# Performance work log

Hardware: AMD Instinct MI355X
Metric: run time of the kernel (lower is better)

The kernel has to match this reference:

```python
import jax, jax.numpy as jnp
import numpy as np
import math

B, T, D = 2, 512, 1024
H, HD = 16, 64
F = 4096
L = 2
R = 32
LOOP_DIM = 64
TEMB = 256
MAXIT = 8
TOPK = 0.55
EPS = 1e-6


def _ste(x, q):
    # straight-through estimator: forward = q, backward = identity
    return x + jax.lax.stop_gradient(q - x)


def bitlinear(x, w, topk_ratio=None):
    # BitNet b1.58 fake-quant: ternary weights (per-tensor absmean scale),
    # int8 per-token absmax activations; optional topk activation sparsity.
    s = jnp.mean(jnp.abs(w)) + 1e-8
    wq = _ste(w, jnp.clip(jnp.round(w / s), -1.0, 1.0) * s)
    if topk_ratio is not None:
        k = max(1, int(math.ceil(topk_ratio * x.shape[-1])))
        ax = jnp.abs(x)
        thr = jax.lax.top_k(ax, k)[0][..., -1:]
        x = jnp.where(ax >= thr, x, 0.0)
    a = jnp.maximum(jnp.max(jnp.abs(x), axis=-1, keepdims=True), 1e-8)
    xq = _ste(x, jnp.clip(jnp.round(x * (127.0 / a)), -128.0, 127.0) * (a / 127.0))
    return xq @ wq.T


def rmsnorm(x, w):
    return x * jax.lax.rsqrt(jnp.mean(x * x, axis=-1, keepdims=True) + EPS) * w


def _rope(x):
    # x: (B,H,T,HD)
    half = HD // 2
    inv = 1.0 / (10000.0 ** (jnp.arange(half, dtype=jnp.float32) / half))
    ang = jnp.arange(x.shape[2], dtype=jnp.float32)[:, None] * inv[None, :]
    cos, sin = jnp.cos(ang), jnp.sin(ang)
    x1, x2 = x[..., :half], x[..., half:]
    return jnp.concatenate([x1 * cos - x2 * sin, x1 * sin + x2 * cos], axis=-1)


def bitblock(h, n1, wq, wk, wv, wo, n2, wg, wu, wd):
    # pre-norm attention + SwiGLU FFN, all projections BitLinear
    b, t, _ = h.shape
    a_in = rmsnorm(h, n1)
    heads = lambda p: p.reshape(b, t, H, HD).transpose(0, 2, 1, 3)
    q = _rope(heads(bitlinear(a_in, wq)))
    k = _rope(heads(bitlinear(a_in, wk)))
    v = heads(bitlinear(a_in, wv))
    scores = jnp.einsum('bhqd,bhkd->bhqk', q, k) / math.sqrt(HD)
    mask = jnp.tril(jnp.ones((t, t), dtype=bool))
    attn = jax.nn.softmax(jnp.where(mask, scores, -1e9), axis=-1)
    o = jnp.einsum('bhqk,bhkd->bhqd', attn, v).transpose(0, 2, 1, 3).reshape(b, t, D)
    h = h + bitlinear(o, wo)
    f_in = rmsnorm(h, n2)
    h = h + bitlinear(jax.nn.silu(bitlinear(f_in, wg)) * bitlinear(f_in, wu), wd)
    return h


def loop_delta(i, t_emb, lp_w, lp2_w, lp2_b):
    # loop_index_inject: sinusoidal loop signal gated by t_emb, padded to D
    half = LOOP_DIM // 2
    frac = i / max(MAXIT - 1, 1)
    freqs = jnp.exp(-math.log(10000.0) * jnp.arange(half, dtype=jnp.float32) / half)
    ang = frac * freqs
    sig = jnp.concatenate([jnp.sin(ang), jnp.cos(ang)])  # (LOOP_DIM,)
    comb = sig[None, :] * (t_emb @ lp_w.T) + (t_emb @ lp2_w.T + lp2_b)  # (B,LOOP_DIM)
    return jnp.pad(comb, ((0, 0), (0, D - LOOP_DIM)))[:, None, :]  # (B,1,D)


def setup_inputs() -> dict:
    key = jax.random.key(0)
    ks = jax.random.split(key, 24)
    g = lambda k, shape, sc=0.02: sc * jax.random.normal(k, shape, dtype=jnp.float32)
    return {
        'x': jax.random.normal(ks[0], (B, T, D), dtype=jnp.float32),
        'e': jax.random.normal(ks[1], (B, T, D), dtype=jnp.float32),
        't_emb': jax.random.normal(ks[2], (B, TEMB), dtype=jnp.float32),
        'blk_norm1': jnp.ones((L, D), jnp.float32),
        'blk_wq': g(ks[3], (L, D, D)),
        'blk_wk': g(ks[4], (L, D, D)),
        'blk_wv': g(ks[5], (L, D, D)),
        'blk_wo': g(ks[6], (L, D, D)),
        'blk_norm2': jnp.ones((L, D), jnp.float32),
        'blk_wg': g(ks[7], (L, F, D)),
        'blk_wu': g(ks[8], (L, F, D)),
        'blk_wd': g(ks[9], (L, D, F)),
        'A_raw': 0.1 * jax.random.normal(ks[10], (D,), dtype=jnp.float32),
        'B_w': g(ks[11], (D, D)),
        'lora_down': g(ks[12], (R, D)),
        'lora_up': g(ks[13], (D, R)),
        'iter_gate': jnp.full((MAXIT,), 0.1, jnp.float32),
        'act_w': g(ks[14], (1, D)),
        'alpha': jnp.full((MAXIT,), 1.0 / L, jnp.float32),
        'loop_proj_w': g(ks[15], (LOOP_DIM, TEMB)),
        'loop_proj2_w': g(ks[16], (LOOP_DIM, TEMB)),
        'loop_proj2_b': jnp.zeros((LOOP_DIM,), jnp.float32),
        'loop_norm_w': jnp.ones((D,), jnp.float32),
        'n_loops': 8,
    }


def reference(x, e, t_emb, blk_norm1, blk_wq, blk_wk, blk_wv, blk_wo,
              blk_norm2, blk_wg, blk_wu, blk_wd, A_raw, B_w,
              lora_down, lora_up, iter_gate, act_w, alpha,
              loop_proj_w, loop_proj2_w, loop_proj2_b, loop_norm_w, n_loops):
    A_eff = 0.99 * jnp.tanh(A_raw)          # diagonal LTI, |A|<0.99
    Be = bitlinear(e, B_w)                  # loop-invariant anchor B(e)
    h = x
    h_out = x
    ws = []
    for i in range(int(n_loops)):
        h_in = rmsnorm(h + loop_delta(i, t_emb, loop_proj_w, loop_proj2_w, loop_proj2_b), loop_norm_w)
        bo = h_in
        for l in range(L):
            bo = bitblock(bo, blk_norm1[l], blk_wq[l], blk_wk[l], blk_wv[l], blk_wo[l],
                          blk_norm2[l], blk_wg[l], blk_wu[l], blk_wd[l])
        bo = alpha[i] * bo
        h = A_eff * h + Be + bo             # LTI injection
        h = h + iter_gate[i] * bitlinear(bitlinear(h, lora_down), lora_up, topk_ratio=TOPK)
        w = jax.nn.sigmoid(bitlinear(h, act_w))  # (B,T,1) soft ACT weight
        h_out = h_out + w * (h - h_out)     # incremental residual blend
        ws.append(w)
    ponder = jnp.mean(jnp.stack(ws))
    return h_out, ponder
```

## Files before the change

### kernel.cpp

```cpp
#include <hip/hip_runtime.h>
#include <stdint.h>

#define DEV static __device__ __forceinline__

typedef float f32x4 __attribute__((ext_vector_type(4)));
typedef int   i32x4 __attribute__((ext_vector_type(4)));
typedef unsigned short u16x8 __attribute__((ext_vector_type(8)));

DEV float bf2f(unsigned short u){ return __uint_as_float(((unsigned int)u)<<16); }
DEV unsigned short f2bfr(float f){
  unsigned int u = __float_as_uint(f);
  return (unsigned short)((u + 0x7FFF + ((u>>16)&1)) >> 16);
}
DEV signed char f2i8(float f){ return (signed char)(int)f; }

DEV float wredsum(float v){
#pragma unroll
  for (int o=32;o;o>>=1) v += __shfl_xor(v,o);
  return v;
}
DEV float wredmax(float v){
#pragma unroll
  for (int o=32;o;o>>=1) v = fmaxf(v,__shfl_xor(v,o));
  return v;
// ... 12 lines not shown
  __syncthreads();
  float r = fmaxf(fmaxf(red[0],red[1]),fmaxf(red[2],red[3]));
  __syncthreads();
  return r;
}

__global__ void fill_k(float* p, int n, float v){
  int i = blockIdx.x*256 + threadIdx.x;
  if (i < n) p[i] = v;
}

__global__ __launch_bounds__(256) void copy_init_k(const float* __restrict__ x,
                                                   float* __restrict__ h, float* __restrict__ ho){
  int i = blockIdx.x*256 + threadIdx.x;
  float4 v = *(const float4*)(x + (size_t)i*4);
  *(float4*)(h  + (size_t)i*4) = v;
  *(float4*)(ho + (size_t)i*4) = v;
  if (blockIdx.x==0 && threadIdx.x==0) ho[1048576] = 0.f;
}

struct WSetup {
  const float* src[18];
  signed char* dst[18];
};
DEV long n4of(int mat){ return mat<9 ? 262144 : (mat<15 ? 1048576 : (mat<17 ? 8192 : 256)); }

__global__ __launch_bounds__(256) void absmean_all_k(WSetup wsu, float* __restrict__ part){
  __shared__ float red[4];
  int mat = blockIdx.x >> 8;
  int seg = blockIdx.x & 255;
  long n4 = n4of(mat);
  const float4* p = (const float4*)wsu.src[mat];
  float s0=0.f, s1=0.f, s2=0.f, s3=0.f;
  long i = (long)seg*256 + threadIdx.x;
  for (; i + 196608 < n4; i += 262144){
    float4 a = p[i], b = p[i+65536], c = p[i+131072], d = p[i+196608];
    s0 += fabsf(a.x)+fabsf(a.y)+fabsf(a.z)+fabsf(a.w);
    s1 += fabsf(b.x)+fabsf(b.y)+fabsf(b.z)+fabsf(b.w);
    s2 += fabsf(c.x)+fabsf(c.y)+fabsf(c.z)+fabsf(c.w);
    s3 += fabsf(d.x)+fabsf(d.y)+fabsf(d.z)+fabsf(d.w);
  }
  for (; i < n4; i += 65536){
    float4 a = p[i];
    s0 += fabsf(a.x)+fabsf(a.y)+fabsf(a.z)+fabsf(a.w);
  }
  float s = bredsum(s0+s1+s2+s3, red);
  if (threadIdx.x==0) part[(long)mat*256 + seg] = s;
}

__global__ __launch_bounds__(256) void finalize_scales_k(const float* __restrict__ part,
                                                         float* __restrict__ scales){
  __shared__ float red[4];
  const long numel[18] = {1048576, 1048576,1048576, 1048576,1048576, 1048576,1048576,
                          1048576,1048576, 4194304,4194304, 4194304,4194304, 4194304,4194304,
                          32768, 32768, 1024};
  for (int m=0;m<18;m++){
    float v = part[(long)m*256 + threadIdx.x];
    v = bredsum(v, red);
    if (threadIdx.x==0) scales[m] = v/(float)numel[m] + 1e-8f;
  }
  if (threadIdx.x==0){
    for (int l=0;l<2;l++){
      scales[18+l*3+0] = scales[1+l];
      scales[18+l*3+1] = scales[3+l];
      scales[18+l*3+2] = scales[5+l];
      scales[24+l*2+0] = scales[9+l];
      scales[24+l*2+1] = scales[11+l];
    }
  }
}

__global__ __launch_bounds__(256) void quantw_all_k(WSetup wsu, const float* __restrict__ scales){
  int bid = blockIdx.x;
  int mat = 0, c = 0;
  for (;;){
    int nb = mat<9 ? 256 : (mat<15 ? 1024 : (mat<17 ? 8 : 1));
    if (bid < c + nb) break;
    c += nb; mat++;
  }
  long seg = bid - c;
  long n4 = n4of(mat);
  float s = scales[mat];
  const float4* src = (const float4*)wsu.src[mat];
  char4* dst = (char4*)wsu.dst[mat];
  long base = seg*1024;
#pragma unroll
  for (int k=0;k<4;k++){
    long i = base + k*256 + threadIdx.x;
    if (i < n4){
      float4 v = src[i];
      char4 q;
      q.x = f2i8(fminf(fmaxf(rintf(v.x/s), -1.f), 1.f));
      q.y = f2i8(fminf(fmaxf(rintf(v.y/s), -1.f), 1.f));
      q.z = f2i8(fminf(fmaxf(rintf(v.z/s), -1.f), 1.f));
      q.w = f2i8(fminf(fmaxf(rintf(v.w/s), -1.f), 1.f));
      dst[i] = q;
    }
  }
}

__global__ __launch_bounds__(256) void delta2_k(const float* __restrict__ temb,
                                                const float* __restrict__ lpw,
                                                const float* __restrict__ lp2w,
                                                const float* __restrict__ lp2b,
                                                float* __restrict__ delta){
  __shared__ float red[4];
  int blk = blockIdx.x;
  int b = blk >> 6, j = blk & 63;
  int t = threadIdx.x;
  float te = temb[b*256 + t];
  float p1 = bredsum(te * lpw[j*256 + t], red);
  float p2 = bredsum(te * lp2w[j*256 + t], red);
  if (t < 8){
    int i = t;
    float frac = (float)i / 7.f;
    int jj = j & 31;
    float fr = expf(-logf(10000.f) * (float)jj * (1.f/32.f));
    float ang = frac * fr;
    float sig = (j < 32) ? sinf(ang) : cosf(ang);
// ... 10 lines not shown
  tab[i*2+1] = sv;
}

__global__ __launch_bounds__(256) void rowquant1k_k(const float* __restrict__ x,
                                                    signed char* __restrict__ xq,
                                                    float* __restrict__ rs){
  __shared__ float red[4];
  int m = blockIdx.x, t = threadIdx.x;
  float v[4];
  float4 f = *(const float4*)(x + (size_t)m*1024 + t*4);
  v[0]=f.x; v[1]=f.y; v[2]=f.z; v[3]=f.w;
  float am = fmaxf(fmaxf(fabsf(v[0]),fabsf(v[1])),fmaxf(fabsf(v[2]),fabsf(v[3])));
  am = bredmax(am, red);
  float a = fmaxf(am, 1e-8f), inv = 127.f/a;
  char4 q;
  q.x = f2i8(fminf(fmaxf(rintf(v[0]*inv),-128.f),127.f));
  q.y = f2i8(fminf(fmaxf(rintf(v[1]*inv),-128.f),127.f));
  q.z = f2i8(fminf(fmaxf(rintf(v[2]*inv),-128.f),127.f));
  q.w = f2i8(fminf(fmaxf(rintf(v[3]*inv),-128.f),127.f));
  *(char4*)(xq + (size_t)m*1024 + t*4) = q;
  if (t==0) rs[m] = a/127.f;
}

__global__ __launch_bounds__(256) void loopnorm_quant_k(const float* __restrict__ h,
                                                        const float* __restrict__ delta,
                                                        const float* __restrict__ lnw,
                                                        const float* __restrict__ n1,
                                                        float* __restrict__ hin,
                                                        signed char* __restrict__ xq,
                                                        float* __restrict__ rs){
  __shared__ float red[4];
  int m = blockIdx.x, t = threadIdx.x;
  int b = m >> 9;
  float v[4];
  float4 f = *(const float4*)(h + (size_t)m*1024 + t*4);
  v[0]=f.x; v[1]=f.y; v[2]=f.z; v[3]=f.w;
  if (t < 16){
#pragma unroll
    for (int j=0;j<4;j++) v[j] += delta[b*64 + t*4 + j];
  }
  float ss = v[0]*v[0]+v[1]*v[1]+v[2]*v[2]+v[3]*v[3];
  ss = bredsum(ss, red);
  float r1 = rsqrtf(ss*(1.f/1024.f) + 1e-6f);
  float w4[4];
#pragma unroll
  for (int j=0;j<4;j++) w4[j] = v[j]*r1*lnw[t*4+j];
  float4 of; of.x=w4[0]; of.y=w4[1]; of.z=w4[2]; of.w=w4[3];
  *(float4*)(hin + (size_t)m*1024 + t*4) = of;
  float s2 = w4[0]*w4[0]+w4[1]*w4[1]+w4[2]*w4[2]+w4[3]*w4[3];
  s2 = bredsum(s2, red);
  float r2 = rsqrtf(s2*(1.f/1024.f) + 1e-6f);
  float y[4];
#pragma unroll
  for (int j=0;j<4;j++) y[j] = w4[j]*r2*n1[t*4+j];
  float am = fmaxf(fmaxf(fabsf(y[0]),fabsf(y[1])),fmaxf(fabsf(y[2]),fabsf(y[3])));
  am = bredmax(am, red);
  float a = fmaxf(am, 1e-8f), inv = 127.f/a;
  char4 q;
  q.x = f2i8(fminf(fmaxf(rintf(y[0]*inv),-128.f),127.f));
  q.y = f2i8(fminf(fmaxf(rintf(y[1]*inv),-128.f),127.f));
  q.z = f2i8(fminf(fmaxf(rintf(y[2]*inv),-128.f),127.f));
  q.w = f2i8(fminf(fmaxf(rintf(y[3]*inv),-128.f),127.f));
  *(char4*)(xq + (size_t)m*1024 + t*4) = q;
  if (t==0) rs[m] = a/127.f;
}

__global__ __launch_bounds__(256) void silu_mul_quant_k(const float* __restrict__ gu,
                                                        signed char* __restrict__ xq,
                                                        float* __restrict__ rs){
  __shared__ float red[4];
  int m = blockIdx.x, t = threadIdx.x;
  const float* g = gu + (size_t)m*8192;
  const float* u = g + 4096;
  float v[16];
#pragma unroll
  for (int j=0;j<16;j+=4){
    float4 gg = *(const float4*)(g + t*16 + j);
    float4 uu = *(const float4*)(u + t*16 + j);
    v[j+0] = gg.x/(1.f+expf(-gg.x))*uu.x;
    v[j+1] = gg.y/(1.f+expf(-gg.y))*uu.y;
    v[j+2] = gg.z/(1.f+expf(-gg.z))*uu.z;
    v[j+3] = gg.w/(1.f+expf(-gg.w))*uu.w;
  }
  float am = 0.f;
#pragma unroll
  for (int j=0;j<16;j++) am = fmaxf(am, fabsf(v[j]));
  am = bredmax(am, red);
  float a = fmaxf(am, 1e-8f), inv = 127.f/a;
#pragma unroll
  for (int j=0;j<16;j+=4){
    char4 q;
    q.x = f2i8(fminf(fmaxf(rintf(v[j+0]*inv),-128.f),127.f));
    q.y = f2i8(fminf(fmaxf(rintf(v[j+1]*inv),-128.f),127.f));
    q.z = f2i8(fminf(fmaxf(rintf(v[j+2]*inv),-128.f),127.f));
    q.w = f2i8(fminf(fmaxf(rintf(v[j+3]*inv),-128.f),127.f));
    *(char4*)(xq + (size_t)m*4096 + t*16 + j) = q;
  }
  if (t==0) rs[m] = a/127.f;
}

DEV f32x4 accfence(f32x4 c){ asm volatile("s_nop 7\n\ts_nop 7" : "+v"(c)); return c; }
DEV i32x4 accfencei(i32x4 c){ asm volatile("s_nop 7\n\ts_nop 7" : "+v"(c)); return c; }

template<int SSHIFT, bool SPLITK>
__global__ __launch_bounds__(256)
void gemm_i8(const signed char* __restrict__ A, const signed char* __restrict__ W,
             const float* __restrict__ rowsc, const float* __restrict__ wscv,
             const float* __restrict__ res, float* __restrict__ C, int N, int Kf, int Kc)
{
  __shared__ __align__(16) signed char As[2][8192];
  __shared__ __align__(16) signed char Bs[2][8192];
  const int tid = threadIdx.x;
  const int lane = tid & 63, wvid = tid >> 6;
  const int wr = wvid >> 1, wc = wvid & 1;
  const int bm = blockIdx.y, bn = blockIdx.x;

  const int r0 = (wvid<<4) + (lane>>2);
  const int sw = (((lane&3) ^ ((r0>>1)&3)) << 4);
  const long kstart = SPLITK ? (long)blockIdx.z * Kc : 0;
  const signed char* gA = A + (size_t)(bm*128 + r0)*Kf + kstart + sw;
  const signed char* gB = W + (size_t)(bn*128 + r0)*Kf + kstart + sw;
  const size_t row64 = (size_t)64*Kf;

#define STAGE(buf, koff) do { \
    __builtin_amdgcn_global_load_lds(gA + (koff),         &As[buf][(wvid<<10)],      16, 0, 0); \
    __builtin_amdgcn_global_load_lds(gA + (koff) + row64, &As[buf][(wvid<<10)+4096], 16, 0, 0); \
    __builtin_amdgcn_global_load_lds(gB + (koff),         &Bs[buf][(wvid<<10)],      16, 0, 0); \
// ... 36 lines not shown
  for (int mi=0;mi<4;mi++)
#pragma unroll
    for (int ni=0;ni<4;ni++)
      acc[mi][ni] = accfencei(acc[mi][ni]);

  const int rif = (lane>>4)<<2;
  const int cif = lane&15;
  const int gcol0 = bn*128 + (wc<<6);

  if constexpr (SPLITK){
    float* P = C + (size_t)blockIdx.z * ((size_t)N << 10);
#pragma unroll
    for (int mi=0;mi<4;mi++)
#pragma unroll
      for (int r=0;r<4;r++){
        const int grow = bm*128 + (wr<<6) + mi*16 + rif + r;
#pragma unroll
        for (int ni=0;ni<4;ni++)
          P[(size_t)grow*N + gcol0 + ni*16 + cif] = (float)acc[mi][ni][r];
      }
    return;
  }

#pragma unroll
  for (int mi=0;mi<4;mi++){
#pragma unroll
    for (int r=0;r<4;r++){
      const int grow = bm*128 + (wr<<6) + mi*16 + rif + r;
      const float rsc = rowsc[grow];
#pragma unroll
      for (int ni=0;ni<4;ni++){
        const int gcol = gcol0 + ni*16 + cif;
        float vvv = (float)acc[mi][ni][r] * rsc * wscv[gcol>>SSHIFT];
        const size_t off = (size_t)grow*N + gcol;
        if (res) vvv += res[off];
        C[off] = vvv;
      }
    }
  }
}

__global__ __launch_bounds__(256) void rope_reduce_k(const float* P,
                                                     const float* __restrict__ rowsc,
                                                     const float* __restrict__ wscv,
                                                     const float* __restrict__ tab,
                                                     float* C){
  int m = blockIdx.x, t = threadIdx.x;
  const float rsc = rowsc[m];
  const int tpos = m & 511;
  const size_t base = (size_t)m*3072;
  const float* P1 = P + 3145728;
  int p0 = t*4;
  int hh = p0 >> 5, d = p0 & 31;
  int c1 = hh*64 + d;
  float wsc = wscv[c1>>10] * rsc;
  float4 xa0 = *(const float4*)(P  + base + c1);
  float4 xa1 = *(const float4*)(P1 + base + c1);
  float4 xb0 = *(const float4*)(P  + base + c1 + 32);
  float4 xb1 = *(const float4*)(P1 + base + c1 + 32);
  float4 cs01 = *(const float4*)(tab + ((size_t)tpos*32 + d)*2);
  float4 cs23 = *(const float4*)(tab + ((size_t)tpos*32 + d)*2 + 4);
  int cv = 2048 + t*4;
  float4 va = *(const float4*)(P  + base + cv);
  float4 vb = *(const float4*)(P1 + base + cv);
  float wv2 = wscv[2] * rsc;

  float x1[4] = {(xa0.x+xa1.x)*wsc, (xa0.y+xa1.y)*wsc, (xa0.z+xa1.z)*wsc, (xa0.w+xa1.w)*wsc};
  float x2[4] = {(xb0.x+xb1.x)*wsc, (xb0.y+xb1.y)*wsc, (xb0.z+xb1.z)*wsc, (xb0.w+xb1.w)*wsc};
  float cc[4] = {cs01.x, cs01.z, cs23.x, cs23.z};
  float ss[4] = {cs01.y, cs01.w, cs23.y, cs23.w};
  float4 o1, o2, ov;
  o1.x = x1[0]*cc[0] - x2[0]*ss[0];  o2.x = x1[0]*ss[0] + x2[0]*cc[0];
  o1.y = x1[1]*cc[1] - x2[1]*ss[1];  o2.y = x1[1]*ss[1] + x2[1]*cc[1];
  o1.z = x1[2]*cc[2] - x2[2]*ss[2];  o2.z = x1[2]*ss[2] + x2[2]*cc[2];
  o1.w = x1[3]*cc[3] - x2[3]*ss[3];  o2.w = x1[3]*ss[3] + x2[3]*cc[3];
  ov.x = (va.x+vb.x)*wv2; ov.y = (va.y+vb.y)*wv2; ov.z = (va.z+vb.z)*wv2; ov.w = (va.w+vb.w)*wv2;
  *(float4*)(C + base + c1)      = o1;
  *(float4*)(C + base + c1 + 32) = o2;
  *(float4*)(C + base + cv)      = ov;
}

__global__ __launch_bounds__(256) void reduce4_k(const float* __restrict__ P,
                                                 const float* __restrict__ rowsc,
                                                 const float* __restrict__ wsc,
                                                 const float* __restrict__ res,
                                                 float* __restrict__ C){
  int m = blockIdx.x, t = threadIdx.x;
  float s0 = rowsc[m] * wsc[0];
  size_t off = (size_t)m*1024 + t*4;
  float4 a = *(const float4*)(P + off);
  float4 b = *(const float4*)(P + 1048576 + off);
  float4 c = *(const float4*)(P + 2097152 + off);
  float4 d = *(const float4*)(P + 3145728 + off);
  float4 o;
  o.x = (a.x+b.x+c.x+d.x)*s0;
  o.y = (a.y+b.y+c.y+d.y)*s0;
  o.z = (a.z+b.z+c.z+d.z)*s0;
  o.w = (a.w+b.w+c.w+d.w)*s0;
  if (res){
    float4 r = *(const float4*)(res + off);
    o.x += r.x; o.y += r.y; o.z += r.z; o.w += r.w;
  }
// ... 38 lines not shown
  q.y = f2i8(fminf(fmaxf(rintf(y[1]*inv),-128.f),127.f));
  q.z = f2i8(fminf(fmaxf(rintf(y[2]*inv),-128.f),127.f));
  q.w = f2i8(fminf(fmaxf(rintf(y[3]*inv),-128.f),127.f));
  *(char4*)(xq + (size_t)m*1024 + t*4) = q;
  if (t==0) rs[m] = aq/127.f;
}

__global__ __launch_bounds__(256) void redfin_k(const float* __restrict__ P,
                                                const float* __restrict__ rowsc,
                                                const float* __restrict__ wsc,
                                                const float* __restrict__ res,
                                                float* __restrict__ h,
                                                const float* __restrict__ Be,
                                                const float* __restrict__ Araw,
                                                const float* __restrict__ alpha, int it,
                                                const signed char* __restrict__ ldq,
                                                const float* __restrict__ sld,
                                                const signed char* __restrict__ luq,
                                                const float* __restrict__ slu,
                                                const signed char* __restrict__ actq,
                                                const float* __restrict__ sact,
                                                const float* __restrict__ ig,
                                                float* __restrict__ hout,
                                                float* __restrict__ ponder){
  __shared__ float red[4];
  __shared__ float xrow[1024];
  __shared__ float part[256];
  __shared__ float xs[32];
  __shared__ float sh_thr, sh_gs;
  int m = blockIdx.x, t = threadIdx.x;
  float al = alpha[it];
  float s0 = rowsc[m] * wsc[0];
  size_t off = (size_t)m*1024 + t*4;
  float4 a = *(const float4*)(P + off);
  float4 b = *(const float4*)(P + 1048576 + off);
  float4 c = *(const float4*)(P + 2097152 + off);
  float4 d = *(const float4*)(P + 3145728 + off);
  float4 r4 = *(const float4*)(res + off);
  float4 hh = *(const float4*)(h + off);
  float4 be = *(const float4*)(Be + off);
  float4 ar = *(const float4*)(Araw + t*4);
  float v[4];
  v[0] = 0.99f*tanhf(ar.x)*hh.x + be.x + al*(r4.x + (a.x+b.x+c.x+d.x)*s0);
  v[1] = 0.99f*tanhf(ar.y)*hh.y + be.y + al*(r4.y + (a.y+b.y+c.y+d.y)*s0);
  v[2] = 0.99f*tanhf(ar.z)*hh.z + be.z + al*(r4.z + (a.z+b.z+c.z+d.z)*s0);
  v[3] = 0.99f*tanhf(ar.w)*hh.w + be.w + al*(r4.w + (a.w+b.w+c.w+d.w)*s0);
  float am = fmaxf(fmaxf(fabsf(v[0]),fabsf(v[1])),fmaxf(fabsf(v[2]),fabsf(v[3])));
// ... 54 lines not shown
    }
    hn[ni] = v[ni] + gs*dd;
  }
  float am2 = fmaxf(fmaxf(fabsf(hn[0]),fabsf(hn[1])),fmaxf(fabsf(hn[2]),fabsf(hn[3])));
  am2 = bredmax(am2, red);
  float a2 = fmaxf(am2, 1e-8f), inv2 = 127.f/a2;
  float zp = 0.f;
#pragma unroll
  for (int ni=0;ni<4;ni++){
    float q = fminf(fmaxf(rintf(hn[ni]*inv2),-128.f),127.f);
    zp += q * (float)actq[n0+ni];
  }
  zp = bredsum(zp, red);
  float z = zp * (a2/127.f) * (*sact);
  float wv = 1.f/(1.f+expf(-z));
#pragma unroll
  for (int ni=0;ni<4;ni++){
    size_t o2 = (size_t)m*1024 + n0+ni;
    float ho = hout[o2];
    hout[o2] = ho + wv*(hn[ni]-ho);
    h[o2] = hn[ni];
  }
  if (t==0) atomicAdd(ponder, wv * (1.f/8192.f));
}

DEV int swz64(int r, int c){ return r*64 + (c ^ ((r&7)<<3)); }
DEV u16x8 cvt8(float4 a, float4 b, float sc){
  u16x8 q;
  q[0]=f2bfr(a.x*sc); q[1]=f2bfr(a.y*sc); q[2]=f2bfr(a.z*sc); q[3]=f2bfr(a.w*sc);
  q[4]=f2bfr(b.x*sc); q[5]=f2bfr(b.y*sc); q[6]=f2bfr(b.z*sc); q[7]=f2bfr(b.w*sc);
  return q;
}

__global__ __launch_bounds__(256) void attn_mfma_k(const float* __restrict__ qkv,
                                                   float* __restrict__ o){
  __shared__ __align__(16) unsigned short Qs[4096];
  __shared__ __align__(16) unsigned short Ks[4096];
  __shared__ __align__(16) unsigned short Vt[4096];
  __shared__ __align__(16) unsigned short Ps[4][1024];
  const int tid = threadIdx.x;
  const int lane = tid & 63, wv = tid >> 6;
  const int qt = blockIdx.x & 7, bh = blockIdx.x >> 3;
  const int b = bh >> 4, h = bh & 15;
  const size_t tokbase = (size_t)(b*512);
  const int l15 = lane & 15, lh = lane >> 4;

  {
    int r = tid >> 2, c0 = (tid & 3) << 4;
    const float* s = qkv + (tokbase + qt*64 + r)*3072 + h*64 + c0;
    float4 f0 = *(const float4*)s,     f1 = *(const float4*)(s+4);
    float4 f2 = *(const float4*)(s+8), f3 = *(const float4*)(s+12);
    *(u16x8*)(Qs + swz64(r, c0))   = cvt8(f0, f1, 0.125f);
    *(u16x8*)(Qs + swz64(r, c0+8)) = cvt8(f2, f3, 0.125f);
  }

  float m_run[4] = {-1e30f,-1e30f,-1e30f,-1e30f};
  float l_run[4] = {0.f,0.f,0.f,0.f};
  f32x4 accO[4] = {};

  for (int kt = 0; kt <= qt; ++kt){
    __syncthreads();
    {
      int r = tid >> 2, c0 = (tid & 3) << 4;
      const float* s = qkv + (tokbase + kt*64 + r)*3072 + 1024 + h*64 + c0;
      float4 f0 = *(const float4*)s,     f1 = *(const float4*)(s+4);
      float4 f2 = *(const float4*)(s+8), f3 = *(const float4*)(s+12);
      *(u16x8*)(Ks + swz64(r, c0))   = cvt8(f0, f1, 1.f);
      *(u16x8*)(Ks + swz64(r, c0+8)) = cvt8(f2, f3, 1.f);
    }
    {
      int r0 = (tid >> 3) << 1, cv = (tid & 7) << 3;
      const float* s0 = qkv + (tokbase + kt*64 + r0)*3072 + 2048 + h*64 + cv;
      const float* s1 = s0 + 3072;
      float4 a0 = *(const float4*)s0, a1 = *(const float4*)(s0+4);
      float4 b0 = *(const float4*)s1, b1 = *(const float4*)(s1+4);
      float va[8] = {a0.x,a0.y,a0.z,a0.w,a1.x,a1.y,a1.z,a1.w};
      float vb[8] = {b0.x,b0.y,b0.z,b0.w,b1.x,b1.y,b1.z,b1.w};
#pragma unroll
      for (int j=0;j<8;j++){
        int d = cv + j;
        unsigned int pk = (unsigned int)f2bfr(va[j]) | ((unsigned int)f2bfr(vb[j])<<16);
        *(unsigned int*)(Vt + swz64(d, r0)) = pk;
      }
    }
    __syncthreads();

    f32x4 s4[4] = {};
#pragma unroll
    for (int kc=0; kc<2; ++kc){
      i32x4 aq = *(const i32x4*)(Qs + swz64(wv*16 + l15, kc*32 + lh*8));
#pragma unroll
      for (int nt=0; nt<4; ++nt){
        i32x4 bk = *(const i32x4*)(Ks + swz64(nt*16 + l15, kc*32 + lh*8));
        asm("v_mfma_f32_16x16x32_bf16 %0, %1, %2, %0" : "+v"(s4[nt]) : "v"(aq), "v"(bk));
      }
    }
#pragma unroll
    for (int nt=0; nt<4; ++nt) s4[nt] = accfence(s4[nt]);

    const bool diag = (kt == qt);
    float sf[4];
#pragma unroll
    for (int r=0;r<4;r++){
      int rl = lh*4 + r;
// ... 14 lines not shown
      m_run[r] = mn;
      float ps = 0.f;
#pragma unroll
      for (int nt=0; nt<4; ++nt){
        float p = __expf(s4[nt][r] - mn);
        ps += p;
        Ps[wv][swz64(rl, nt*16 + l15)] = f2bfr(p);
      }
      ps += __shfl_xor(ps,1); ps += __shfl_xor(ps,2);
      ps += __shfl_xor(ps,4); ps += __shfl_xor(ps,8);
      l_run[r] = l_run[r]*sf[r] + ps;
    }
#pragma unroll
    for (int dt=0; dt<4; ++dt){
#pragma unroll
      for (int r=0;r<4;r++) accO[dt][r] *= sf[r];
      accO[dt] = accfence(accO[dt]);
    }
#pragma unroll
    for (int kc=0; kc<2; ++kc){
      i32x4 pa = *(const i32x4*)(Ps[wv] + swz64(l15, kc*32 + lh*8));
#pragma unroll
      for (int dt=0; dt<4; ++dt){
        i32x4 vb2 = *(const i32x4*)(Vt + swz64(dt*16 + l15, kc*32 + lh*8));
        asm("v_mfma_f32_16x16x32_bf16 %0, %1, %2, %0" : "+v"(accO[dt]) : "v"(pa), "v"(vb2));
      }
    }
  }
#pragma unroll
  for (int dt=0; dt<4; ++dt) accO[dt] = accfence(accO[dt]);
#pragma unroll
  for (int r=0;r<4;r++){
    float invl = 1.f / l_run[r];
    int row = qt*64 + wv*16 + lh*4 + r;
    float* op = o + (tokbase + row)*1024 + h*64 + l15;
#pragma unroll
    for (int dt=0; dt<4; ++dt)
      op[dt*16] = accO[dt][r] * invl;
  }
}

extern "C" void kernel_launch(void* const* d_in, const int* in_sizes, int n_in,
                              void* d_out, int out_size, void* d_ws, size_t ws_size,
                              hipStream_t stream)
{
  (void)in_sizes; (void)n_in;
  const float* x     = (const float*)d_in[0];
  const float* e     = (const float*)d_in[1];
  const float* temb  = (const float*)d_in[2];
  const float* bn1   = (const float*)d_in[3];
  const float* bwq   = (const float*)d_in[4];
  const float* bwk   = (const float*)d_in[5];
  const float* bwv   = (const float*)d_in[6];
  const float* bwo   = (const float*)d_in[7];
  const float* bn2   = (const float*)d_in[8];
  const float* bwg   = (const float*)d_in[9];
  const float* bwu   = (const float*)d_in[10];
  const float* bwd   = (const float*)d_in[11];
// ... 13 lines not shown
  float* out = (float*)d_out;
  const size_t WS_NEEDED = 94600704ull;
  if (ws_size < WS_NEEDED){
    fill_k<<<(out_size+255)/256,256,0,stream>>>(out, out_size, 1.0e9f);
    return;
  }

  signed char* qw_qkv = (signed char*)(ws + 0);
  signed char* qw_wo  = (signed char*)(ws + 6291456);
  signed char* qw_gu  = (signed char*)(ws + 8388608);
  signed char* qw_wd  = (signed char*)(ws + 25165824);
  signed char* qw_bw  = (signed char*)(ws + 33554432);
  signed char* qw_ld  = (signed char*)(ws + 34603008);
  signed char* qw_lu  = (signed char*)(ws + 34635776);
  signed char* qw_act = (signed char*)(ws + 34668544);
  float* scales = (float*)(ws + 34669568);
  float* part   = (float*)(ws + 34670080);
  float* delta  = (float*)(ws + 34688512);
  float* hbuf   = (float*)(ws + 34692608);
  float* Bebuf  = (float*)(ws + 38886912);
  float* bufX   = (float*)(ws + 43081216);
  float* bufY   = (float*)(ws + 47275520);
  float* gub    = (float*)(ws + 51469824);
  float* qkvb   = gub;
  float* obuf   = (float*)(ws + 85024256);
  signed char* xq1k = (signed char*)(ws + 89218560);
  float* rs1k   = (float*)(ws + 90267136);
  signed char* xqm  = (signed char*)(ws + 90271232);
  float* rsm    = (float*)(ws + 94465536);
  float* ropetab= (float*)(ws + 94469632);

  WSetup wsu;
  wsu.src[0]=Bw;
  wsu.src[1]=bwq; wsu.src[2]=bwq+1048576;
  wsu.src[3]=bwk; wsu.src[4]=bwk+1048576;
  wsu.src[5]=bwv; wsu.src[6]=bwv+1048576;
  wsu.src[7]=bwo; wsu.src[8]=bwo+1048576;
  wsu.src[9]=bwg; wsu.src[10]=bwg+4194304;
  wsu.src[11]=bwu; wsu.src[12]=bwu+4194304;
  wsu.src[13]=bwd; wsu.src[14]=bwd+4194304;
  wsu.src[15]=ldw; wsu.src[16]=luw; wsu.src[17]=actw;
  wsu.dst[0]=qw_bw;
  wsu.dst[1]=qw_qkv;             wsu.dst[2]=qw_qkv+3145728;
  wsu.dst[3]=qw_qkv+1048576;     wsu.dst[4]=qw_qkv+3145728+1048576;
  wsu.dst[5]=qw_qkv+2097152;     wsu.dst[6]=qw_qkv+3145728+2097152;
  wsu.dst[7]=qw_wo;              wsu.dst[8]=qw_wo+1048576;
  wsu.dst[9]=qw_gu;              wsu.dst[10]=qw_gu+8388608;
  wsu.dst[11]=qw_gu+4194304;     wsu.dst[12]=qw_gu+8388608+4194304;
  wsu.dst[13]=qw_wd;             wsu.dst[14]=qw_wd+4194304;
  wsu.dst[15]=qw_ld; wsu.dst[16]=qw_lu; wsu.dst[17]=qw_act;

  absmean_all_k<<<4608,256,0,stream>>>(wsu, part);
  finalize_scales_k<<<1,256,0,stream>>>(part, scales);
  quantw_all_k<<<8465,256,0,stream>>>(wsu, scales);

  delta2_k<<<128,256,0,stream>>>(temb, lpw, lp2w, lp2b, delta);
  ropetab_k<<<64,256,0,stream>>>(ropetab);
  copy_init_k<<<1024,256,0,stream>>>(x, hbuf, out);

  rowquant1k_k<<<1024,256,0,stream>>>(e, xq1k, rs1k);
  { dim3 g(8,8,4); gemm_i8<0,true><<<g,256,0,stream>>>(xq1k, qw_bw, nullptr, nullptr, nullptr, gub, 1024, 1024, 256); }
  reduce4_k<<<1024,256,0,stream>>>(gub, rs1k, scales+0, nullptr, Bebuf);

  for (int it=0; it<8; ++it){
    loopnorm_quant_k<<<1024,256,0,stream>>>(hbuf, delta + it*128, lnw, bn1, bufX, xq1k, rs1k);
    for (int l=0;l<2;l++){
      { dim3 g(24,8,2); gemm_i8<0,true><<<g,256,0,stream>>>(xq1k, qw_qkv + (size_t)l*3145728, nullptr, nullptr, nullptr, gub, 3072, 1024, 512); }
      rope_reduce_k<<<1024,256,0,stream>>>(gub, rs1k, scales+18+l*3, ropetab, qkvb);
      attn_mfma_k<<<256,256,0,stream>>>(qkvb, obuf);
      rowquant1k_k<<<1024,256,0,stream>>>(obuf, xq1k, rs1k);
      { dim3 g(8,8,4); gemm_i8<0,true><<<g,256,0,stream>>>(xq1k, qw_wo + (size_t)l*1048576, nullptr, nullptr, nullptr, gub, 1024, 1024, 256); }
      redq_norm_k<<<1024,256,0,stream>>>(gub, rs1k, scales+7+l, bufX, bn2 + (size_t)l*1024, bufY, xq1k, rs1k);
      { dim3 g(64,8); gemm_i8<12,false><<<g,256,0,stream>>>(xq1k, qw_gu + (size_t)l*8388608, rs1k, scales+24+l*2, nullptr, gub, 8192, 1024, 1024); }
      silu_mul_quant_k<<<1024,256,0,stream>>>(gub, xqm, rsm);
      { dim3 g(8,8,4); gemm_i8<0,true><<<g,256,0,stream>>>(xqm, qw_wd + (size_t)l*4194304, nullptr, nullptr, nullptr, gub, 1024, 4096, 1024); }
      if (l==0){
        redq_norm_k<<<1024,256,0,stream>>>(gub, rsm, scales+13, bufY, bn1 + 1024, bufX, xq1k, rs1k);
      } else {
        redfin_k<<<1024,256,0,stream>>>(gub, rsm, scales+14, bufY, hbuf, Bebuf, Araw, alph, it,
                                        qw_ld, scales+15, qw_lu, scales+16, qw_act, scales+17,
                                        ig, out, out + 1048576);
      }
    }
  }
}
```

Baseline: 2.111 ms.

## Fuse RoPE into attention, SiLU into gate/up GEMM, loopnorm into final reduce

Fuses RoPE and the split-K reduction into the attention kernel, so the separate rope_reduce pass and its intermediate buffer disappear. The gate and up weights are interleaved row by row so the gate/up GEMM epilogue can apply SiLU times up via a lane shuffle, writing a 4096-wide result that only needs row quantisation. The next iteration's loop-norm and quantisation are fused into the tail of redfin_k, and the absmean reduction now reads contiguous segments per block. Together these cut launches and global memory round trips, at the cost of extra per-element work in the attention load phase and a half-lane store pattern in the GEMM epilogue.

Result: slower. 2.243 ms (+6.3%).

```diff
diff --git a/kernel.cpp b/kernel.cpp
--- a/kernel.cpp
+++ b/kernel.cpp
@@ -58,6 +58,7 @@
 struct WSetup {
   const float* src[18];
   signed char* dst[18];
+  int mode[18];
 };
 DEV long n4of(int mat){ return mat<9 ? 262144 : (mat<15 ? 1048576 : (mat<17 ? 8192 : 256)); }
 
@@ -66,18 +67,19 @@
   int mat = blockIdx.x >> 8;
   int seg = blockIdx.x & 255;
   long n4 = n4of(mat);
-  const float4* p = (const float4*)wsu.src[mat];
+  long cnt = n4 >> 8;
+  const float4* p = (const float4*)wsu.src[mat] + (long)seg*cnt;
   float s0=0.f, s1=0.f, s2=0.f, s3=0.f;
-  long i = (long)seg*256 + threadIdx.x;
-  for (; i + 196608 < n4; i += 262144){
-    float4 a = p[i], b = p[i+65536], c = p[i+131072], d = p[i+196608];
+  long j = threadIdx.x;
+  for (; j + 768 < cnt; j += 1024){
+    float4 a = p[j], b = p[j+256], c = p[j+512], d = p[j+768];
     s0 += fabsf(a.x)+fabsf(a.y)+fabsf(a.z)+fabsf(a.w);
     s1 += fabsf(b.x)+fabsf(b.y)+fabsf(b.z)+fabsf(b.w);
     s2 += fabsf(c.x)+fabsf(c.y)+fabsf(c.z)+fabsf(c.w);
     s3 += fabsf(d.x)+fabsf(d.y)+fabsf(d.z)+fabsf(d.w);
   }
-  for (; i < n4; i += 65536){
-    float4 a = p[i];
+  for (; j < cnt; j += 256){
+    float4 a = p[j];
     s0 += fabsf(a.x)+fabsf(a.y)+fabsf(a.z)+fabsf(a.w);
   }
   float s = bredsum(s0+s1+s2+s3, red);
@@ -117,6 +119,7 @@
   long seg = bid - c;
   long n4 = n4of(mat);
   float s = scales[mat];
+  int md = wsu.mode[mat];
   const float4* src = (const float4*)wsu.src[mat];
   char4* dst = (char4*)wsu.dst[mat];
   long base = seg*1024;
@@ -130,7 +133,11 @@
       q.y = f2i8(fminf(fmaxf(rintf(v.y/s), -1.f), 1.f));
       q.z = f2i8(fminf(fmaxf(rintf(v.z/s), -1.f), 1.f));
       q.w = f2i8(fminf(fmaxf(rintf(v.w/s), -1.f), 1.f));
-      dst[i] = q;
+      if (md == 0) dst[i] = q;
+      else {
+        long r = i >> 8, cc = i & 255;
+        dst[(((r<<1) | (md-1))<<8) | cc] = q;
+      }
     }
   }
 }
@@ -187,6 +194,35 @@
   if (t==0) rs[m] = a/127.f;
 }
 
+__global__ __launch_bounds__(256) void rowquant4k_k(const float* __restrict__ x,
+                                                    signed char* __restrict__ xq,
+                                                    float* __restrict__ rs){
+  __shared__ float red[4];
+  int m = blockIdx.x, t = threadIdx.x;
+  const float* p = x + (size_t)m*4096 + t*16;
+  float v[16];
+#pragma unroll
+  for (int j=0;j<16;j+=4){
+    float4 f = *(const float4*)(p + j);
+    v[j]=f.x; v[j+1]=f.y; v[j+2]=f.z; v[j+3]=f.w;
+  }
+  float am = 0.f;
+#pragma unroll
+  for (int j=0;j<16;j++) am = fmaxf(am, fabsf(v[j]));
+  am = bredmax(am, red);
+  float a = fmaxf(am, 1e-8f), inv = 127.f/a;
+#pragma unroll
+  for (int j=0;j<16;j+=4){
+    char4 q;
+    q.x = f2i8(fminf(fmaxf(rintf(v[j+0]*inv),-128.f),127.f));
+    q.y = f2i8(fminf(fmaxf(rintf(v[j+1]*inv),-128.f),127.f));
+    q.z = f2i8(fminf(fmaxf(rintf(v[j+2]*inv),-128.f),127.f));
+    q.w = f2i8(fminf(fmaxf(rintf(v[j+3]*inv),-128.f),127.f));
+    *(char4*)(xq + (size_t)m*4096 + t*16 + j) = q;
+  }
+  if (t==0) rs[m] = a/127.f;
+}
+
 __global__ __launch_bounds__(256) void loopnorm_quant_k(const float* __restrict__ h,
                                                         const float* __restrict__ delta,
                                                         const float* __restrict__ lnw,
@@ -230,44 +266,10 @@
   if (t==0) rs[m] = a/127.f;
 }
 
-__global__ __launch_bounds__(256) void silu_mul_quant_k(const float* __restrict__ gu,
-                                                        signed char* __restrict__ xq,
-                                                        float* __restrict__ rs){
-  __shared__ float red[4];
-  int m = blockIdx.x, t = threadIdx.x;
-  const float* g = gu + (size_t)m*8192;
-  const float* u = g + 4096;
-  float v[16];
-#pragma unroll
-  for (int j=0;j<16;j+=4){
-    float4 gg = *(const float4*)(g + t*16 + j);
-    float4 uu = *(const float4*)(u + t*16 + j);
-    v[j+0] = gg.x/(1.f+expf(-gg.x))*uu.x;
-    v[j+1] = gg.y/(1.f+expf(-gg.y))*uu.y;
-    v[j+2] = gg.z/(1.f+expf(-gg.z))*uu.z;
-    v[j+3] = gg.w/(1.f+expf(-gg.w))*uu.w;
-  }
-  float am = 0.f;
-#pragma unroll
-  for (int j=0;j<16;j++) am = fmaxf(am, fabsf(v[j]));
-  am = bredmax(am, red);
-  float a = fmaxf(am, 1e-8f), inv = 127.f/a;
-#pragma unroll
-  for (int j=0;j<16;j+=4){
-    char4 q;
-    q.x = f2i8(fminf(fmaxf(rintf(v[j+0]*inv),-128.f),127.f));
-    q.y = f2i8(fminf(fmaxf(rintf(v[j+1]*inv),-128.f),127.f));
-    q.z = f2i8(fminf(fmaxf(rintf(v[j+2]*inv),-128.f),127.f));
-    q.w = f2i8(fminf(fmaxf(rintf(v[j+3]*inv),-128.f),127.f));
-    *(char4*)(xq + (size_t)m*4096 + t*16 + j) = q;
-  }
-  if (t==0) rs[m] = a/127.f;
-}
-
 DEV f32x4 accfence(f32x4 c){ asm volatile("s_nop 7\n\ts_nop 7" : "+v"(c)); return c; }
 DEV i32x4 accfencei(i32x4 c){ asm volatile("s_nop 7\n\ts_nop 7" : "+v"(c)); return c; }
 
-template<int SSHIFT, bool SPLITK>
+template<bool SPLITK, bool GUSILU>
 __global__ __launch_bounds__(256)
 void gemm_i8(const signed char* __restrict__ A, const signed char* __restrict__ W,
              const float* __restrict__ rowsc, const float* __restrict__ wscv,
@@ -350,6 +352,30 @@
     return;
   }
 
+  if constexpr (GUSILU){
+    const float sg = wscv[0], su = wscv[1];
+#pragma unroll
+    for (int mi=0;mi<4;mi++){
+#pragma unroll
+      for (int r=0;r<4;r++){
+        const int grow = bm*128 + (wr<<6) + mi*16 + rif + r;
+        const float rsc = rowsc[grow];
+#pragma unroll
+        for (int ni=0;ni<4;ni++){
+          const int gcol = gcol0 + ni*16 + cif;
+          float val = (float)acc[mi][ni][r] * rsc * ((gcol & 1) ? su : sg);
+          float other = __shfl_xor(val, 1);
+          if (!(lane & 1)){
+            float g = val, u = other;
+            float outv = g/(1.f+expf(-g))*u;
+            C[(size_t)grow*4096 + (gcol>>1)] = outv;
+          }
+        }
+      }
+    }
+    return;
+  }
+
 #pragma unroll
   for (int mi=0;mi<4;mi++){
 #pragma unroll
@@ -359,53 +385,13 @@
 #pragma unroll
       for (int ni=0;ni<4;ni++){
         const int gcol = gcol0 + ni*16 + cif;
-        float vvv = (float)acc[mi][ni][r] * rsc * wscv[gcol>>SSHIFT];
+        float vvv = (float)acc[mi][ni][r] * rsc * wscv[0];
         const size_t off = (size_t)grow*N + gcol;
         if (res) vvv += res[off];
         C[off] = vvv;
       }
     }
   }
-}
-
-__global__ __launch_bounds__(256) void rope_reduce_k(const float* P,
-                                                     const float* __restrict__ rowsc,
-                                                     const float* __restrict__ wscv,
-                                                     const float* __restrict__ tab,
-                                                     float* C){
-  int m = blockIdx.x, t = threadIdx.x;
-  const float rsc = rowsc[m];
-  const int tpos = m & 511;
-  const size_t base = (size_t)m*3072;
-  const float* P1 = P + 3145728;
-  int p0 = t*4;
-  int hh = p0 >> 5, d = p0 & 31;
-  int c1 = hh*64 + d;
-  float wsc = wscv[c1>>10] * rsc;
-  float4 xa0 = *(const float4*)(P  + base + c1);
-  float4 xa1 = *(const float4*)(P1 + base + c1);
-  float4 xb0 = *(const float4*)(P  + base + c1 + 32);
-  float4 xb1 = *(const float4*)(P1 + base + c1 + 32);
-  float4 cs01 = *(const float4*)(tab + ((size_t)tpos*32 + d)*2);
-  float4 cs23 = *(const float4*)(tab + ((size_t)tpos*32 + d)*2 + 4);
-  int cv = 2048 + t*4;
-  float4 va = *(const float4*)(P  + base + cv);
-  float4 vb = *(const float4*)(P1 + base + cv);
-  float wv2 = wscv[2] * rsc;
-
-  float x1[4] = {(xa0.x+xa1.x)*wsc, (xa0.y+xa1.y)*wsc, (xa0.z+xa1.z)*wsc, (xa0.w+xa1.w)*wsc};
-  float x2[4] = {(xb0.x+xb1.x)*wsc, (xb0.y+xb1.y)*wsc, (xb0.z+xb1.z)*wsc, (xb0.w+xb1.w)*wsc};
-  float cc[4] = {cs01.x, cs01.z, cs23.x, cs23.z};
-  float ss[4] = {cs01.y, cs01.w, cs23.y, cs23.w};
-  float4 o1, o2, ov;
-  o1.x = x1[0]*cc[0] - x2[0]*ss[0];  o2.x = x1[0]*ss[0] + x2[0]*cc[0];
-  o1.y = x1[1]*cc[1] - x2[1]*ss[1];  o2.y = x1[1]*ss[1] + x2[1]*cc[1];
-  o1.z = x1[2]*cc[2] - x2[2]*ss[2];  o2.z = x1[2]*ss[2] + x2[2]*cc[2];
-  o1.w = x1[3]*cc[3] - x2[3]*ss[3];  o2.w = x1[3]*ss[3] + x2[3]*cc[3];
-  ov.x = (va.x+vb.x)*wv2; ov.y = (va.y+vb.y)*wv2; ov.z = (va.z+vb.z)*wv2; ov.w = (va.w+vb.w)*wv2;
-  *(float4*)(C + base + c1)      = o1;
-  *(float4*)(C + base + c1 + 32) = o2;
-  *(float4*)(C + base + cv)      = ov;
 }
 
 __global__ __launch_bounds__(256) void reduce4_k(const float* __restrict__ P,
@@ -490,7 +476,14 @@
                                                 const float* __restrict__ sact,
                                                 const float* __restrict__ ig,
                                                 float* __restrict__ hout,
-                                                float* __restrict__ ponder){
+                                                float* __restrict__ ponder,
+                                                const float* __restrict__ dnext,
+                                                const float* __restrict__ lnw,
+                                                const float* __restrict__ n1,
+                                                float* __restrict__ hin,
+                                                signed char* __restrict__ xqn,
+                                                float* __restrict__ rsn,
+                                                int doNext){
   __shared__ float red[4];
   __shared__ float xrow[1024];
   __shared__ float part[256];
@@ -591,18 +584,54 @@
     h[o2] = hn[ni];
   }
   if (t==0) atomicAdd(ponder, wv * (1.f/8192.f));
+
+  if (doNext){
+    int b2 = m >> 9;
+    float v2[4] = {hn[0], hn[1], hn[2], hn[3]};
+    if (t < 16){
+#pragma unroll
+      for (int j=0;j<4;j++) v2[j] += dnext[b2*64 + t*4 + j];
+    }
+    float ss2 = v2[0]*v2[0]+v2[1]*v2[1]+v2[2]*v2[2]+v2[3]*v2[3];
+    ss2 = bredsum(ss2, red);
+    float r1 = rsqrtf(ss2*(1.f/1024.f) + 1e-6f);
+    float w4[4];
+#pragma unroll
+    for (int j=0;j<4;j++) w4[j] = v2[j]*r1*lnw[t*4+j];
+    float4 of; of.x=w4[0]; of.y=w4[1]; of.z=w4[2]; of.w=w4[3];
+    *(float4*)(hin + off) = of;
+    float s2 = w4[0]*w4[0]+w4[1]*w4[1]+w4[2]*w4[2]+w4[3]*w4[3];
+    s2 = bredsum(s2, red);
+    float r2 = rsqrtf(s2*(1.f/1024.f) + 1e-6f);
+    float y[4];
+#pragma unroll
+    for (int j=0;j<4;j++) y[j] = w4[j]*r2*n1[t*4+j];
+    float am3 = fmaxf(fmaxf(fabsf(y[0]),fabsf(y[1])),fmaxf(fabsf(y[2]),fabsf(y[3])));
+    am3 = bredmax(am3, red);
+    float aq3 = fmaxf(am3, 1e-8f), inv3 = 127.f/aq3;
+    char4 q;
+    q.x = f2i8(fminf(fmaxf(rintf(y[0]*inv3),-128.f),127.f));
+    q.y = f2i8(fminf(fmaxf(rintf(y[1]*inv3),-128.f),127.f));
+    q.z = f2i8(fminf(fmaxf(rintf(y[2]*inv3),-128.f),127.f));
+    q.w = f2i8(fminf(fmaxf(rintf(y[3]*inv3),-128.f),127.f));
+    *(char4*)(xqn + off) = q;
+    if (t==0) rsn[m] = aq3/127.f;
+  }
 }
 
 DEV int swz64(int r, int c){ return r*64 + (c ^ ((r&7)<<3)); }
-DEV u16x8 cvt8(float4 a, float4 b, float sc){
-  u16x8 q;
-  q[0]=f2bfr(a.x*sc); q[1]=f2bfr(a.y*sc); q[2]=f2bfr(a.z*sc); q[3]=f2bfr(a.w*sc);
-  q[4]=f2bfr(b.x*sc); q[5]=f2bfr(b.y*sc); q[6]=f2bfr(b.z*sc); q[7]=f2bfr(b.w*sc);
-  return q;
-}
-
-__global__ __launch_bounds__(256) void attn_mfma_k(const float* __restrict__ qkv,
-                                                   float* __restrict__ o){
+DEV void ld8sum(const float* __restrict__ p0, const float* __restrict__ p1, float sc, float* x){
+  float4 a0 = *(const float4*)p0, a1 = *(const float4*)(p0+4);
+  float4 b0 = *(const float4*)p1, b1 = *(const float4*)(p1+4);
+  x[0]=(a0.x+b0.x)*sc; x[1]=(a0.y+b0.y)*sc; x[2]=(a0.z+b0.z)*sc; x[3]=(a0.w+b0.w)*sc;
+  x[4]=(a1.x+b1.x)*sc; x[5]=(a1.y+b1.y)*sc; x[6]=(a1.z+b1.z)*sc; x[7]=(a1.w+b1.w)*sc;
+}
+
+__global__ __launch_bounds__(256) void attn_fused_k(const float* __restrict__ P,
+                                                    const float* __restrict__ rs,
+                                                    const float* __restrict__ sc3,
+                                                    const float* __restrict__ tab,
+                                                    float* __restrict__ o){
   __shared__ __align__(16) unsigned short Qs[4096];
   __shared__ __align__(16) unsigned short Ks[4096];
   __shared__ __align__(16) unsigned short Vt[4096];
@@ -611,16 +640,31 @@
   const int lane = tid & 63, wv = tid >> 6;
   const int qt = blockIdx.x & 7, bh = blockIdx.x >> 3;
   const int b = bh >> 4, h = bh & 15;
-  const size_t tokbase = (size_t)(b*512);
+  const int tokb = b*512;
   const int l15 = lane & 15, lh = lane >> 4;
+  const float* P1 = P + 3145728;
+  const float sq = sc3[0]*0.125f, sk = sc3[1], sv = sc3[2];
 
   {
-    int r = tid >> 2, c0 = (tid & 3) << 4;
-    const float* s = qkv + (tokbase + qt*64 + r)*3072 + h*64 + c0;
-    float4 f0 = *(const float4*)s,     f1 = *(const float4*)(s+4);
-    float4 f2 = *(const float4*)(s+8), f3 = *(const float4*)(s+12);
-    *(u16x8*)(Qs + swz64(r, c0))   = cvt8(f0, f1, 0.125f);
-    *(u16x8*)(Qs + swz64(r, c0+8)) = cvt8(f2, f3, 0.125f);
+    int r = tid >> 2, d0 = (tid & 3) << 3;
+    int m = tokb + qt*64 + r;
+    float rsc = rs[m] * sq;
+    const float* p0 = P  + (size_t)m*3072 + h*64;
+    const float* p1 = P1 + (size_t)m*3072 + h*64;
+    float x1[8], x2[8];
+    ld8sum(p0+d0,    p1+d0,    rsc, x1);
+    ld8sum(p0+d0+32, p1+d0+32, rsc, x2);
+    int tpos = qt*64 + r;
+    const float* cs = tab + ((size_t)(tpos*32 + d0))*2;
+    u16x8 lo, hi;
+#pragma unroll
+    for (int k2=0;k2<8;k2++){
+      float cv = cs[2*k2], sn = cs[2*k2+1];
+      lo[k2] = f2bfr(x1[k2]*cv - x2[k2]*sn);
+      hi[k2] = f2bfr(x1[k2]*sn + x2[k2]*cv);
+    }
+    *(u16x8*)(Qs + swz64(r, d0))    = lo;
+    *(u16x8*)(Qs + swz64(r, d0+32)) = hi;
   }
 
   float m_run[4] = {-1e30f,-1e30f,-1e30f,-1e30f};
@@ -630,25 +674,39 @@
   for (int kt = 0; kt <= qt; ++kt){
     __syncthreads();
     {
-      int r = tid >> 2, c0 = (tid & 3) << 4;
-      const float* s = qkv + (tokbase + kt*64 + r)*3072 + 1024 + h*64 + c0;
-      float4 f0 = *(const float4*)s,     f1 = *(const float4*)(s+4);
-      float4 f2 = *(const float4*)(s+8), f3 = *(const float4*)(s+12);
-      *(u16x8*)(Ks + swz64(r, c0))   = cvt8(f0, f1, 1.f);
-      *(u16x8*)(Ks + swz64(r, c0+8)) = cvt8(f2, f3, 1.f);
+      int r = tid >> 2, d0 = (tid & 3) << 3;
+      int m = tokb + kt*64 + r;
+      float rsc = rs[m] * sk;
+      const float* p0 = P  + (size_t)m*3072 + 1024 + h*64;
+      const float* p1 = P1 + (size_t)m*3072 + 1024 + h*64;
+      float x1[8], x2[8];
+      ld8sum(p0+d0,    p1+d0,    rsc, x1);
+      ld8sum(p0+d0+32, p1+d0+32, rsc, x2);
+      int tpos = kt*64 + r;
+      const float* cs = tab + ((size_t)(tpos*32 + d0))*2;
+      u16x8 lo, hi;
+#pragma unroll
+      for (int k2=0;k2<8;k2++){
+        float cv = cs[2*k2], sn = cs[2*k2+1];
+        lo[k2] = f2bfr(x1[k2]*cv - x2[k2]*sn);
+        hi[k2] = f2bfr(x1[k2]*sn + x2[k2]*cv);
+      }
+      *(u16x8*)(Ks + swz64(r, d0))    = lo;
+      *(u16x8*)(Ks + swz64(r, d0+32)) = hi;
     }
     {
       int r0 = (tid >> 3) << 1, cv = (tid & 7) << 3;
-      const float* s0 = qkv + (tokbase + kt*64 + r0)*3072 + 2048 + h*64 + cv;
-      const float* s1 = s0 + 3072;
-      float4 a0 = *(const float4*)s0, a1 = *(const float4*)(s0+4);
-      float4 b0 = *(const float4*)s1, b1 = *(const float4*)(s1+4);
-      float va[8] = {a0.x,a0.y,a0.z,a0.w,a1.x,a1.y,a1.z,a1.w};
-      float vb[8] = {b0.x,b0.y,b0.z,b0.w,b1.x,b1.y,b1.z,b1.w};
+      int m0 = tokb + kt*64 + r0;
+      float rsc0 = rs[m0]*sv, rsc1 = rs[m0+1]*sv;
+      const float* q0 = P  + (size_t)m0*3072 + 2048 + h*64 + cv;
+      const float* q1 = P1 + (size_t)m0*3072 + 2048 + h*64 + cv;
+      float va[8], vb2[8];
+      ld8sum(q0,      q1,      rsc0, va);
+      ld8sum(q0+3072, q1+3072, rsc1, vb2);
 #pragma unroll
       for (int j=0;j<8;j++){
         int d = cv + j;
-        unsigned int pk = (unsigned int)f2bfr(va[j]) | ((unsigned int)f2bfr(vb[j])<<16);
+        unsigned int pk = (unsigned int)f2bfr(va[j]) | ((unsigned int)f2bfr(vb2[j])<<16);
         *(unsigned int*)(Vt + swz64(d, r0)) = pk;
       }
     }
@@ -709,8 +767,8 @@
       i32x4 pa = *(const i32x4*)(Ps[wv] + swz64(l15, kc*32 + lh*8));
 #pragma unroll
       for (int dt=0; dt<4; ++dt){
-        i32x4 vb2 = *(const i32x4*)(Vt + swz64(dt*16 + l15, kc*32 + lh*8));
-        asm("v_mfma_f32_16x16x32_bf16 %0, %1, %2, %0" : "+v"(accO[dt]) : "v"(pa), "v"(vb2));
+        i32x4 vb3 = *(const i32x4*)(Vt + swz64(dt*16 + l15, kc*32 + lh*8));
+        asm("v_mfma_f32_16x16x32_bf16 %0, %1, %2, %0" : "+v"(accO[dt]) : "v"(pa), "v"(vb3));
       }
     }
   }
@@ -720,7 +778,7 @@
   for (int r=0;r<4;r++){
     float invl = 1.f / l_run[r];
     int row = qt*64 + wv*16 + lh*4 + r;
-    float* op = o + (tokbase + row)*1024 + h*64 + l15;
+    float* op = o + (size_t)(tokb + row)*1024 + h*64 + l15;
 #pragma unroll
     for (int dt=0; dt<4; ++dt)
       op[dt*16] = accO[dt][r] * invl;
@@ -780,7 +838,6 @@
   float* bufX   = (float*)(ws + 43081216);
   float* bufY   = (float*)(ws + 47275520);
   float* gub    = (float*)(ws + 51469824);
-  float* qkvb   = gub;
   float* obuf   = (float*)(ws + 85024256);
   signed char* xq1k = (signed char*)(ws + 89218560);
   float* rs1k   = (float*)(ws + 90267136);
@@ -804,9 +861,12 @@
   wsu.dst[5]=qw_qkv+2097152;     wsu.dst[6]=qw_qkv+3145728+2097152;
   wsu.dst[7]=qw_wo;              wsu.dst[8]=qw_wo+1048576;
   wsu.dst[9]=qw_gu;              wsu.dst[10]=qw_gu+8388608;
-  wsu.dst[11]=qw_gu+4194304;     wsu.dst[12]=qw_gu+8388608+4194304;
+  wsu.dst[11]=qw_gu;             wsu.dst[12]=qw_gu+8388608;
   wsu.dst[13]=qw_wd;             wsu.dst[14]=qw_wd+4194304;
   wsu.dst[15]=qw_ld; wsu.dst[16]=qw_lu; wsu.dst[17]=qw_act;
+  for (int i=0;i<18;i++) wsu.mode[i]=0;
+  wsu.mode[9]=1;  wsu.mode[10]=1;
+  wsu.mode[11]=2; wsu.mode[12]=2;
 
   absmean_all_k<<<4608,256,0,stream>>>(wsu, part);
   finalize_scales_k<<<1,256,0,stream>>>(part, scales);
@@ -817,28 +877,30 @@
   copy_init_k<<<1024,256,0,stream>>>(x, hbuf, out);
 
   rowquant1k_k<<<1024,256,0,stream>>>(e, xq1k, rs1k);
-  { dim3 g(8,8,4); gemm_i8<0,true><<<g,256,0,stream>>>(xq1k, qw_bw, nullptr, nullptr, nullptr, gub, 1024, 1024, 256); }
+  { dim3 g(8,8,4); gemm_i8<true,false><<<g,256,0,stream>>>(xq1k, qw_bw, nullptr, nullptr, nullptr, gub, 1024, 1024, 256); }
   reduce4_k<<<1024,256,0,stream>>>(gub, rs1k, scales+0, nullptr, Bebuf);
 
   for (int it=0; it<8; ++it){
-    loopnorm_quant_k<<<1024,256,0,stream>>>(hbuf, delta + it*128, lnw, bn1, bufX, xq1k, rs1k);
+    if (it==0)
+      loopnorm_quant_k<<<1024,256,0,stream>>>(hbuf, delta, lnw, bn1, bufX, xq1k, rs1k);
     for (int l=0;l<2;l++){
-      { dim3 g(24,8,2); gemm_i8<0,true><<<g,256,0,stream>>>(xq1k, qw_qkv + (size_t)l*3145728, nullptr, nullptr, nullptr, gub, 3072, 1024, 512); }
-      rope_reduce_k<<<1024,256,0,stream>>>(gub, rs1k, scales+18+l*3, ropetab, qkvb);
-      attn_mfma_k<<<256,256,0,stream>>>(qkvb, obuf);
+      { dim3 g(24,8,2); gemm_i8<true,false><<<g,256,0,stream>>>(xq1k, qw_qkv + (size_t)l*3145728, nullptr, nullptr, nullptr, gub, 3072, 1024, 512); }
+      attn_fused_k<<<256,256,0,stream>>>(gub, rs1k, scales+18+l*3, ropetab, obuf);
       rowquant1k_k<<<1024,256,0,stream>>>(obuf, xq1k, rs1k);
-      { dim3 g(8,8,4); gemm_i8<0,true><<<g,256,0,stream>>>(xq1k, qw_wo + (size_t)l*1048576, nullptr, nullptr, nullptr, gub, 1024, 1024, 256); }
+      { dim3 g(8,8,4); gemm_i8<true,false><<<g,256,0,stream>>>(xq1k, qw_wo + (size_t)l*1048576, nullptr, nullptr, nullptr, gub, 1024, 1024, 256); }
       redq_norm_k<<<1024,256,0,stream>>>(gub, rs1k, scales+7+l, bufX, bn2 + (size_t)l*1024, bufY, xq1k, rs1k);
-      { dim3 g(64,8); gemm_i8<12,false><<<g,256,0,stream>>>(xq1k, qw_gu + (size_t)l*8388608, rs1k, scales+24+l*2, nullptr, gub, 8192, 1024, 1024); }
-      silu_mul_quant_k<<<1024,256,0,stream>>>(gub, xqm, rsm);
-      { dim3 g(8,8,4); gemm_i8<0,true><<<g,256,0,stream>>>(xqm, qw_wd + (size_t)l*4194304, nullptr, nullptr, nullptr, gub, 1024, 4096, 1024); }
+      { dim3 g(64,8); gemm_i8<false,true><<<g,256,0,stream>>>(xq1k, qw_gu + (size_t)l*8388608, rs1k, scales+24+l*2, nullptr, gub, 8192, 1024, 1024); }
+      rowquant4k_k<<<1024,256,0,stream>>>(gub, xqm, rsm);
+      { dim3 g(8,8,4); gemm_i8<true,false><<<g,256,0,stream>>>(xqm, qw_wd + (size_t)l*4194304, nullptr, nullptr, nullptr, gub, 1024, 4096, 1024); }
       if (l==0){
         redq_norm_k<<<1024,256,0,stream>>>(gub, rsm, scales+13, bufY, bn1 + 1024, bufX, xq1k, rs1k);
       } else {
         redfin_k<<<1024,256,0,stream>>>(gub, rsm, scales+14, bufY, hbuf, Bebuf, Araw, alph, it,
                                         qw_ld, scales+15, qw_lu, scales+16, qw_act, scales+17,
-                                        ig, out, out + 1048576);
-      }
-    }
-  }
-}
+                                        ig, out, out + 1048576,
+                                        delta + (it+1 < 8 ? (it+1)*128 : 0), lnw, bn1, bufX, xq1k, rs1k,
+                                        (it < 7) ? 1 : 0);
+      }
+    }
+  }
+}
```
